# Kernel optimization log

Measured on AMD Instinct MI355X. Metric: run time of the kernel, lower is better.

Reference implementation:

```python
import jax, jax.numpy as jnp
import numpy as np

SEQ = 4096
EMBED = 1280
HEADS = 16
HEAD_DIM = EMBED // HEADS  # 80


def rotate_half(x):
    # interleaved rotate: out[..., 2i] = -x[..., 2i+1]; out[..., 2i+1] = x[..., 2i]
    x_even = x[..., ::2]
    x_odd = x[..., 1::2]
    return jnp.stack((-x_odd, x_even), axis=-1).reshape(x.shape)


def setup_inputs() -> dict:
    key = jax.random.key(0)
    ks = jax.random.split(key, 7)
    return {
        "hidden_states": jax.random.normal(ks[0], (SEQ, EMBED), dtype=jnp.float32),
        "cos": jax.random.uniform(ks[1], (SEQ, HEAD_DIM), dtype=jnp.float32),
        "sin": jax.random.uniform(ks[2], (SEQ, HEAD_DIM), dtype=jnp.float32),
        "w_qkv": jax.random.normal(ks[3], (EMBED, 3 * EMBED), dtype=jnp.float32) * 0.02,
        "b_qkv": jax.random.normal(ks[4], (3 * EMBED,), dtype=jnp.float32) * 0.02,
        "w_proj": jax.random.normal(ks[5], (EMBED, EMBED), dtype=jnp.float32) * 0.02,
        "b_proj": jax.random.normal(ks[6], (EMBED,), dtype=jnp.float32) * 0.02,
    }


def reference(hidden_states, cos, sin, w_qkv, b_qkv, w_proj, b_proj):
    S = hidden_states.shape[0]
    # QKV projection: (S, 3E) -> (S, 3, H, D)
    qkv = (hidden_states @ w_qkv + b_qkv).reshape(S, 3, HEADS, HEAD_DIM)
    q, k, v = qkv[:, 0], qkv[:, 1], qkv[:, 2]  # each (S, H, D)

    # RoPE in float32, cos/sin broadcast over heads: (S, 1, D)
    dt = q.dtype
    qf, kf = q.astype(jnp.float32), k.astype(jnp.float32)
    c = cos[:, None, :].astype(jnp.float32)
    s = sin[:, None, :].astype(jnp.float32)
    q = (qf * c + rotate_half(qf) * s).astype(dt)
    k = (kf * c + rotate_half(kf) * s).astype(dt)

    scaling = HEAD_DIM ** -0.5
    # attention scores per head: (H, S, S)
    scores = jnp.einsum("shd,thd->hst", q, k) * scaling
    attn = jax.nn.softmax(scores.astype(jnp.float32), axis=-1).astype(dt)
    # weighted values: (S, H, D)
    out = jnp.einsum("hst,thd->shd", attn, v).reshape(S, EMBED)
    return out @ w_proj + b_proj
```

## Files before the change

### kernel.cpp

```cpp
#include <hip/hip_runtime.h>
#include <hip/hip_bf16.h>

#define SEQ   4096
#define EMBED 1280
#define NH    16
#define HD    80
#define K1    EMBED
#define N1    (3*EMBED)

typedef short bfrag_t __attribute__((ext_vector_type(8)));
typedef float f32x4   __attribute__((ext_vector_type(4)));
typedef float f32x16  __attribute__((ext_vector_type(16)));

static __device__ __forceinline__ unsigned short f2bf(float x){
    __hip_bfloat16 h = __float2bfloat16(x);
    return __builtin_bit_cast(unsigned short, h);
}
static __device__ __forceinline__ float bf2f(unsigned short u){
    unsigned int v = ((unsigned int)u) << 16;
    return __builtin_bit_cast(float, v);
}

static __device__ __forceinline__ unsigned int pack2bf(float a, float b){
    unsigned int ua = __builtin_bit_cast(unsigned int, a) + 0x8000u;
    unsigned int ub = __builtin_bit_cast(unsigned int, b) + 0x8000u;
#if __has_builtin(__builtin_amdgcn_perm)
    return __builtin_amdgcn_perm(ub, ua, 0x07060302u);
#else
    return (ua >> 16) | (ub & 0xFFFF0000u);
#endif
}

static __device__ __forceinline__ float fast_exp2(float x){
#if __has_builtin(__builtin_amdgcn_exp2f)
    return __builtin_amdgcn_exp2f(x);
#else
    return __expf(x * 0.69314718056f);
#endif
}

static __device__ __forceinline__ void gload_lds16(const void* g, void* l){
#if __has_builtin(__builtin_amdgcn_global_load_lds)
    __builtin_amdgcn_global_load_lds(
        (const __attribute__((address_space(1))) unsigned int*)g,
        (__attribute__((address_space(3))) unsigned int*)l, 16, 0, 0);
#else
    *(uint4*)l = *(const uint4*)g;
#endif
}

static __device__ __forceinline__ bfrag_t ld_frag8(const unsigned short* p){
    uint2 lo = *(const uint2*)p;
    uint2 hi = *(const uint2*)(p + 4);
    uint4 u; u.x = lo.x; u.y = lo.y; u.z = hi.x; u.w = hi.y;
    return __builtin_bit_cast(bfrag_t, u);
}

#define CONV_BLOCKS (SEQ*EMBED/4/256)
#define TQ_BX (N1/32)
#define TQ_BLOCKS (TQ_BX*(K1/32))
#define TP_BX (EMBED/32)
#define TP_BLOCKS (TP_BX*(EMBED/32))

__global__ __launch_bounds__(256)
void prep_all(const float* __restrict__ hs, unsigned short* __restrict__ hb,
              const float* __restrict__ wqkv, unsigned short* __restrict__ wqT,
              const float* __restrict__ wproj, unsigned short* __restrict__ wpT)
{
    __shared__ float t[32][33];
    int b = blockIdx.x;
    if (b < CONV_BLOCKS){
        int i = b * 256 + threadIdx.x;
        float4 v = ((const float4*)hs)[i];
        ushort4 r;
        r.x = f2bf(v.x); r.y = f2bf(v.y); r.z = f2bf(v.z); r.w = f2bf(v.w);
        ((ushort4*)hb)[i] = r;
        return;
    }
    const float* in; unsigned short* outp; int R, C, bc, br;
    if (b < CONV_BLOCKS + TQ_BLOCKS){
        b -= CONV_BLOCKS;
        in = wqkv; outp = wqT; R = K1; C = N1;
        bc = (b % TQ_BX) * 32; br = (b / TQ_BX) * 32;
    } else {
        b -= CONV_BLOCKS + TQ_BLOCKS;
        in = wproj; outp = wpT; R = EMBED; C = EMBED;
        bc = (b % TP_BX) * 32; br = (b / TP_BX) * 32;
    }
    int tx = threadIdx.x & 31, ty = threadIdx.x >> 5;
    for (int i = ty; i < 32; i += 8) t[i][tx] = in[(size_t)(br + i) * C + bc + tx];
    __syncthreads();
    for (int i = ty; i < 32; i += 8) outp[(size_t)(bc + i) * R + br + tx] = f2bf(t[tx][i]);
}


__global__ __launch_bounds__(256, 4)
void gemm_qkv(const unsigned short* __restrict__ A,
              const unsigned short* __restrict__ BT,
              const float* __restrict__ bias,
              const float* __restrict__ cosp, const float* __restrict__ sinp,
              unsigned short* __restrict__ qout, unsigned short* __restrict__ kout,
              unsigned short* __restrict__ vout,
              int M, int N, int K)
{
    __shared__ union {
        struct { unsigned short A[128*32]; unsigned short B[128*32]; } ab;
        unsigned short tr[4][64][72];
    } lds;

    int tid  = threadIdx.x;
    int lane = tid & 63, wave = tid >> 6;
    int wm = wave >> 1, wn = wave & 1;
    int quad = lane >> 4, l16 = lane & 15;
    int m0 = blockIdx.y * 128, n0 = blockIdx.x * 128;

    f32x4 acc[4][4] = {};
    const unsigned short* ga = A  + (size_t)(m0 + (tid>>2)) * K + (tid&3)*8;
    const unsigned short* gb = BT + (size_t)(n0 + (tid>>2)) * K + (tid&3)*8;

    for (int k0 = 0; k0 < K; k0 += 32){
        __syncthreads();
        gload_lds16(ga,                &lds.ab.A[tid*8]);
        gload_lds16(ga + (size_t)64*K, &lds.ab.A[2048 + tid*8]);
        gload_lds16(gb,                &lds.ab.B[tid*8]);
        gload_lds16(gb + (size_t)64*K, &lds.ab.B[2048 + tid*8]);
        ga += 32; gb += 32;
        __syncthreads();
        bfrag_t af[4], bf[4];
        #pragma unroll
        for (int i = 0; i < 4; i++)
            af[i] = *(const bfrag_t*)&lds.ab.A[(wm*64 + i*16 + l16)*32 + quad*8];
        #pragma unroll
        for (int j = 0; j < 4; j++)
            bf[j] = *(const bfrag_t*)&lds.ab.B[(wn*64 + j*16 + l16)*32 + quad*8];
        #pragma unroll
        for (int i = 0; i < 4; i++)
            #pragma unroll
            for (int j = 0; j < 4; j++)
                acc[i][j] = __builtin_amdgcn_mfma_f32_16x16x32_bf16(af[i], bf[j], acc[i][j], 0, 0, 0);
    }

    const float scaling = 0.11180339887498949f;

    if (n0 >= 2*EMBED){
        __syncthreads();
        #pragma unroll
        for (int j = 0; j < 4; j++){
            int colw = j*16 + l16;
            float b = bias[n0 + wn*64 + colw];
            #pragma unroll
            for (int i = 0; i < 4; i++){
                ushort4 u;
                u.x = f2bf(acc[i][j][0] + b);
                u.y = f2bf(acc[i][j][1] + b);
                u.z = f2bf(acc[i][j][2] + b);
                u.w = f2bf(acc[i][j][3] + b);
                *(ushort4*)&lds.tr[wave][colw][i*16 + quad*4] = u;
            }
        }
        int c8 = lane >> 3, rc = lane & 7;
        #pragma unroll
        for (int cg = 0; cg < 8; cg++){
            int colw = cg*8 + c8;
            size_t colg = (size_t)(n0 - 2*EMBED) + wn*64 + colw;
            int rowg = m0 + wm*64 + rc*8;
            *(uint4*)&vout[colg*SEQ + rowg] = *(const uint4*)&lds.tr[wave][colw][rc*8];
        }
        return;
    }

    #pragma unroll
    for (int i = 0; i < 4; i++)
    #pragma unroll
    for (int j = 0; j < 4; j++){
        int colj  = n0 + wn*64 + j*16;
        int which = colj / EMBED;
        int rem   = colj - which*EMBED;
        int hh    = rem / HD;
        int dd    = rem - hh*HD;
        float b = bias[colj + l16];
        unsigned short* dst = (which == 0) ? qout : kout;
        float mult = (which == 0) ? scaling : 1.f;
        #pragma unroll
        for (int r = 0; r < 4; r++){
            int row = m0 + wm*64 + i*16 + quad*4 + r;
            float v = acc[i][j][r] + b;
            float vo = __shfl_xor(v, 1, 64);
            float c = cosp[(size_t)row*HD + dd + l16];
            float s = sinp[(size_t)row*HD + dd + l16];
            float o = (l16 & 1) ? (v*c + vo*s) : (v*c - vo*s);
            dst[((size_t)hh*SEQ + row)*HD + dd + l16] = f2bf(o * mult);
        }
    }
}


__global__ __launch_bounds__(256, 4)
void gemm_proj(const unsigned short* __restrict__ A,
               const unsigned short* __restrict__ BT,
               const float* __restrict__ bias,
               float* __restrict__ out,
               int M, int N, int K)
{
    __shared__ unsigned short As[64*32];
    __shared__ unsigned short Bs[128*32];
    int tid  = threadIdx.x;
    int lane = tid & 63, wave = tid >> 6;
    int wm = wave & 1, wn = wave >> 1;
    int quad = lane >> 4, l16 = lane & 15;
    int m0 = blockIdx.y * 64, n0 = blockIdx.x * 128;

    f32x4 acc[2][4] = {};
    const unsigned short* ga = A  + (size_t)(m0 + (tid>>2)) * K + (tid&3)*8;
    const unsigned short* gb = BT + (size_t)(n0 + (tid>>2)) * K + (tid&3)*8;

    for (int k0 = 0; k0 < K; k0 += 32){
        __syncthreads();
        gload_lds16(ga,                &As[tid*8]);
        gload_lds16(gb,                &Bs[tid*8]);
        gload_lds16(gb + (size_t)64*K, &Bs[2048 + tid*8]);
        ga += 32; gb += 32;
        __syncthreads();
        bfrag_t af[2], bf[4];
        #pragma unroll
        for (int i = 0; i < 2; i++)
            af[i] = *(const bfrag_t*)&As[(wm*32 + i*16 + l16)*32 + quad*8];
        #pragma unroll
        for (int j = 0; j < 4; j++)
            bf[j] = *(const bfrag_t*)&Bs[(wn*64 + j*16 + l16)*32 + quad*8];
        #pragma unroll
        for (int i = 0; i < 2; i++)
            #pragma unroll
            for (int j = 0; j < 4; j++)
                acc[i][j] = __builtin_amdgcn_mfma_f32_16x16x32_bf16(af[i], bf[j], acc[i][j], 0, 0, 0);
    }

    #pragma unroll
    for (int i = 0; i < 2; i++)
    #pragma unroll
    for (int j = 0; j < 4; j++){
        int col = n0 + wn*64 + j*16 + l16;
        float b = bias[col];
        #pragma unroll
        for (int r = 0; r < 4; r++){
            int row = m0 + wm*32 + i*16 + quad*4 + r;
            out[(size_t)row * N + col] = acc[i][j][r] + b;
        }
    }
}


__global__ __launch_bounds__(256, 4)
void attn_mfma(const unsigned short* __restrict__ q,
               const unsigned short* __restrict__ k,
               const unsigned short* __restrict__ vt,
               unsigned short* __restrict__ out,
               unsigned short* __restrict__ opart,
               float* __restrict__ lpart,
               int iters)
{
    __shared__ unsigned short Vt[2][80*64];
    __shared__ unsigned short Ps[128][68];

    int tid  = threadIdx.x;
    int lane = tid & 63, wave = tid >> 6;
    int quad = lane >> 4, l16 = lane & 15;
    int l32  = lane & 31, h2 = lane >> 5;
    int h = blockIdx.y, q0 = blockIdx.x * 128;
    int split = blockIdx.z;
    int kb0 = split * iters * 64;
    int qrow = wave*32 + l32;

    const unsigned short* qh = q  + ((size_t)h*SEQ + q0)*HD;
    const unsigned short* kh = k  + (size_t)h*SEQ*HD;
    const unsigned short* vh = vt + (size_t)h*HD*SEQ;

    bfrag_t qf[5];
    #pragma unroll
    for (int kk = 0; kk < 5; kk++)
        qf[kk] = *(const bfrag_t*)&qh[(size_t)qrow*HD + (kk*2 + h2)*8];

    auto stage = [&](int buf, int kb){
        unsigned short* dst = &Vt[buf][0];
        #pragma unroll
        for (int rnd = 0; rnd < 3; rnd++){
            int idx = rnd*256 + tid;
            if (rnd < 2 || tid < 128){
                int row = idx >> 3, c = idx & 7;
                gload_lds16(&vh[(size_t)row*SEQ + kb + ((c ^ (row & 7)) << 3)], &dst[idx*8]);
            }
        }
    };

    stage(0, kb0);

    float la = 0.f, lb = 0.f;
    f32x4 o_[2][5] = {};

    const unsigned short* kp = kh + (size_t)(kb0 + l32)*HD + h2*8;
    const float LOG2E = 1.44269504f;
    const float BIAS2 = -17.3123405f;

    for (int kt = 0; kt < iters; kt++){
        f32x16 S0 = {}, S1 = {};
        #pragma unroll
        for (int kk = 0; kk < 5; kk++){
            bfrag_t kf0 = *(const bfrag_t*)(kp + kk*16);
            bfrag_t kf1 = *(const bfrag_t*)(kp + (size_t)32*HD + kk*16);
            S0 = __builtin_amdgcn_mfma_f32_32x32x16_bf16(kf0, qf[kk], S0, 0,0,0);
            S1 = __builtin_amdgcn_mfma_f32_32x32x16_bf16(kf1, qf[kk], S1, 0,0,0);
        }
        kp += (size_t)64*HD;

        #pragma unroll
        for (int r = 0; r < 16; r++){
            float p0 = fast_exp2(fmaf(S0[r], LOG2E, BIAS2));
            float p1 = fast_exp2(fmaf(S1[r], LOG2E, BIAS2));
            S0[r] = p0; S1[r] = p1;
            la += p0; lb += p1;
        }

        #pragma unroll
        for (int g = 0; g < 4; g++){
            uint2 w0, w1;
            w0.x = pack2bf(S0[g*4+0], S0[g*4+1]);
            w0.y = pack2bf(S0[g*4+2], S0[g*4+3]);
            w1.x = pack2bf(S1[g*4+0], S1[g*4+1]);
            w1.y = pack2bf(S1[g*4+2], S1[g*4+3]);
            *(uint2*)&Ps[qrow][g*8 + h2*4]      = w0;
            *(uint2*)&Ps[qrow][32 + g*8 + h2*4] = w1;
        }

        __syncthreads();
        if (kt + 1 < iters) stage((kt+1)&1, kb0 + (kt+1)*64);

        int buf = kt & 1;
        #pragma unroll
        for (int kk = 0; kk < 2; kk++){
            bfrag_t pf0 = ld_frag8(&Ps[wave*32      + l16][kk*32 + quad*8]);
            bfrag_t pf1 = ld_frag8(&Ps[wave*32 + 16 + l16][kk*32 + quad*8]);
            #pragma unroll
            for (int dt = 0; dt < 5; dt++){
                int row = dt*16 + l16;
                bfrag_t vf = *(const bfrag_t*)&Vt[buf][row*64 + (((kk*4+quad) ^ (l16 & 7)) << 3)];
                o_[0][dt] = __builtin_amdgcn_mfma_f32_16x16x32_bf16(vf, pf0, o_[0][dt], 0,0,0);
                o_[1][dt] = __builtin_amdgcn_mfma_f32_16x16x32_bf16(vf, pf1, o_[1][dt], 0,0,0);
            }
        }
    }

    float l_ = la + lb;
    l_ += __shfl_xor(l_, 32, 64);

    if (gridDim.z == 1){
        #pragma unroll
        for (int i = 0; i < 2; i++){
            float linv = 1.f / __shfl(l_, i*16 + l16, 64);
            int qg = q0 + wave*32 + i*16 + l16;
            #pragma unroll
            for (int dt = 0; dt < 5; dt++){
                int d = dt*16 + quad*4;
                ushort4 u;
                u.x = f2bf(o_[i][dt][0]*linv);
                u.y = f2bf(o_[i][dt][1]*linv);
                u.z = f2bf(o_[i][dt][2]*linv);
                u.w = f2bf(o_[i][dt][3]*linv);
                *(ushort4*)&out[(size_t)qg*EMBED + h*HD + d] = u;
            }
        }
    } else {
        if (h2 == 0)
            lpart[((size_t)(split*NH + h))*SEQ + q0 + qrow] = l_;
        #pragma unroll
        for (int i = 0; i < 2; i++){
            int qg = q0 + wave*32 + i*16 + l16;
            size_t base = (((size_t)(split*NH + h))*SEQ + qg)*HD;
            #pragma unroll
            for (int dt = 0; dt < 5; dt++){
                int d = dt*16 + quad*4;
                ushort4 u;
                u.x = f2bf(o_[i][dt][0]);
                u.y = f2bf(o_[i][dt][1]);
                u.z = f2bf(o_[i][dt][2]);
                u.w = f2bf(o_[i][dt][3]);
                *(ushort4*)&opart[base + d] = u;
            }
        }
    }
}

__global__ __launch_bounds__(256)
void attn_combine(const unsigned short* __restrict__ op,
                  const float* __restrict__ lp,
                  unsigned short* __restrict__ out,
                  int ns)
{
    int t = blockIdx.x*256 + threadIdx.x;
    int d8 = t % 10;
    int qh = t / 10;
    int q  = qh & (SEQ-1);
    int h  = qh >> 12;
    float lsum = 0.f;
    for (int s = 0; s < ns; s++) lsum += lp[((size_t)(s*NH + h))*SEQ + q];
    float inv = 1.f / lsum;
    float acc[8] = {};
    for (int s = 0; s < ns; s++){
        uint4 A = *(const uint4*)&op[(((size_t)(s*NH + h))*SEQ + q)*HD + d8*8];
        unsigned int* a = (unsigned int*)&A;
        #pragma unroll
        for (int e = 0; e < 4; e++){
            acc[2*e]   += bf2f((unsigned short)(a[e] & 0xffff));
            acc[2*e+1] += bf2f((unsigned short)(a[e] >> 16));
        }
    }
    uint4 R;
    unsigned int* r = (unsigned int*)&R;
    #pragma unroll
    for (int e = 0; e < 4; e++)
        r[e] = pack2bf(acc[2*e]*inv, acc[2*e+1]*inv);
    *(uint4*)&out[(size_t)q*EMBED + h*HD + d8*8] = R;
}


extern "C" void kernel_launch(void* const* d_in, const int* in_sizes, int n_in,
                              void* d_out, int out_size, void* d_ws, size_t ws_size,
                              hipStream_t stream)
{
    const float* hs    = (const float*)d_in[0];
    const float* cosp  = (const float*)d_in[1];
    const float* sinp  = (const float*)d_in[2];
    const float* wqkv  = (const float*)d_in[3];
    const float* bqkv  = (const float*)d_in[4];
    const float* wproj = (const float*)d_in[5];
    const float* bproj = (const float*)d_in[6];
    float* out = (float*)d_out;

    char* ws = (char*)d_ws;
    size_t off = 0;
    auto alloc = [&](size_t bytes){ void* p = ws + off; off += bytes; return p; };
    unsigned short* hb    = (unsigned short*)alloc((size_t)SEQ*EMBED*2);
    unsigned short* wqT   = (unsigned short*)alloc((size_t)N1*K1*2);
    unsigned short* wpT   = (unsigned short*)alloc((size_t)EMBED*EMBED*2);
    unsigned short* q_ws  = (unsigned short*)alloc((size_t)SEQ*EMBED*2);
    unsigned short* k_ws  = (unsigned short*)alloc((size_t)SEQ*EMBED*2);
    unsigned short* v_ws  = (unsigned short*)alloc((size_t)SEQ*EMBED*2);
    unsigned short* a_ws  = (unsigned short*)alloc((size_t)SEQ*EMBED*2);
    size_t base = off;
    size_t per_split = (size_t)NH*SEQ*HD*2 + (size_t)NH*SEQ*4;
    int nsplit = 1;
    if (ws_size >= base + 4*per_split)      nsplit = 4;
    else if (ws_size >= base + 2*per_split) nsplit = 2;
    unsigned short* opart = (unsigned short*)alloc((size_t)nsplit*NH*SEQ*HD*2);
    float*          lpart = (float*)alloc((size_t)nsplit*NH*SEQ*4);

    prep_all<<<CONV_BLOCKS + TQ_BLOCKS + TP_BLOCKS, 256, 0, stream>>>(
        hs, hb, wqkv, wqT, wproj, wpT);

    gemm_qkv<<<dim3(N1/128, SEQ/128), 256, 0, stream>>>(
        hb, wqT, bqkv, cosp, sinp, q_ws, k_ws, v_ws, SEQ, N1, K1);

    attn_mfma<<<dim3(SEQ/128, NH, nsplit), 256, 0, stream>>>(
        q_ws, k_ws, v_ws, a_ws, opart, lpart, (SEQ/64)/nsplit);
    if (nsplit > 1)
        attn_combine<<<NH*SEQ*10/256, 256, 0, stream>>>(opart, lpart, a_ws, nsplit);

    gemm_proj<<<dim3(EMBED/128, SEQ/64), 256, 0, stream>>>(
        a_ws, wpT, bproj, out, SEQ, EMBED, EMBED);
}
```

Baseline: 322.6 us.

## Widen QKV GEMM K-tile to 64 with XOR-swizzled LDS, cap attention split at 2

The QKV GEMM now stages a 64-wide K slice per iteration instead of 32. This halves the number of barrier pairs, and an XOR swizzle on the LDS column index avoids bank conflicts on fragment reads. Separately, pack2bf uses the hardware packed bf16 conversion when available, and the attention split-K factor is capped at 2 instead of 4. Together these aim to cut GEMM synchronisation overhead and combine-kernel work. The trade-offs are doubled LDS use for the GEMM tiles, which may lower occupancy, and less parallelism in attention.

```diff
diff --git a/kernel.cpp b/kernel.cpp
--- a/kernel.cpp
+++ b/kernel.cpp
@@ -22,12 +22,17 @@
 }
 
 static __device__ __forceinline__ unsigned int pack2bf(float a, float b){
+#if __has_builtin(__builtin_amdgcn_cvt_pk_bf16_f32)
+    short2 p = __builtin_amdgcn_cvt_pk_bf16_f32(a, b);
+    return __builtin_bit_cast(unsigned int, p);
+#else
     unsigned int ua = __builtin_bit_cast(unsigned int, a) + 0x8000u;
     unsigned int ub = __builtin_bit_cast(unsigned int, b) + 0x8000u;
 #if __has_builtin(__builtin_amdgcn_perm)
     return __builtin_amdgcn_perm(ub, ua, 0x07060302u);
 #else
     return (ua >> 16) | (ub & 0xFFFF0000u);
+#endif
 #endif
 }
 
@@ -104,7 +109,7 @@
               int M, int N, int K)
 {
     __shared__ union {
-        struct { unsigned short A[128*32]; unsigned short B[128*32]; } ab;
+        struct { unsigned short A[128*64]; unsigned short B[128*64]; } ab;
         unsigned short tr[4][64][72];
     } lds;
 
@@ -114,30 +119,49 @@
     int quad = lane >> 4, l16 = lane & 15;
     int m0 = blockIdx.y * 128, n0 = blockIdx.x * 128;
 
+    const unsigned short* pa[4];
+    const unsigned short* pb[4];
+    int dsto[4];
+    #pragma unroll
+    for (int rnd = 0; rnd < 4; rnd++){
+        int idx = rnd*256 + tid;
+        int row = idx >> 3, c = idx & 7;
+        int cc = (c ^ (row & 7)) * 8;
+        pa[rnd] = A  + (size_t)(m0 + row) * K + cc;
+        pb[rnd] = BT + (size_t)(n0 + row) * K + cc;
+        dsto[rnd] = idx * 8;
+    }
+
     f32x4 acc[4][4] = {};
-    const unsigned short* ga = A  + (size_t)(m0 + (tid>>2)) * K + (tid&3)*8;
-    const unsigned short* gb = BT + (size_t)(n0 + (tid>>2)) * K + (tid&3)*8;
-
-    for (int k0 = 0; k0 < K; k0 += 32){
-        __syncthreads();
-        gload_lds16(ga,                &lds.ab.A[tid*8]);
-        gload_lds16(ga + (size_t)64*K, &lds.ab.A[2048 + tid*8]);
-        gload_lds16(gb,                &lds.ab.B[tid*8]);
-        gload_lds16(gb + (size_t)64*K, &lds.ab.B[2048 + tid*8]);
-        ga += 32; gb += 32;
-        __syncthreads();
-        bfrag_t af[4], bf[4];
-        #pragma unroll
-        for (int i = 0; i < 4; i++)
-            af[i] = *(const bfrag_t*)&lds.ab.A[(wm*64 + i*16 + l16)*32 + quad*8];
-        #pragma unroll
-        for (int j = 0; j < 4; j++)
-            bf[j] = *(const bfrag_t*)&lds.ab.B[(wn*64 + j*16 + l16)*32 + quad*8];
-        #pragma unroll
-        for (int i = 0; i < 4; i++)
-            #pragma unroll
-            for (int j = 0; j < 4; j++)
-                acc[i][j] = __builtin_amdgcn_mfma_f32_16x16x32_bf16(af[i], bf[j], acc[i][j], 0, 0, 0);
+
+    for (int k0 = 0; k0 < K; k0 += 64){
+        __syncthreads();
+        #pragma unroll
+        for (int rnd = 0; rnd < 4; rnd++){
+            gload_lds16(pa[rnd], &lds.ab.A[dsto[rnd]]);
+            gload_lds16(pb[rnd], &lds.ab.B[dsto[rnd]]);
+            pa[rnd] += 64; pb[rnd] += 64;
+        }
+        __syncthreads();
+        #pragma unroll
+        for (int kk = 0; kk < 2; kk++){
+            bfrag_t af[4], bf[4];
+            #pragma unroll
+            for (int i = 0; i < 4; i++){
+                int row = wm*64 + i*16 + l16;
+                af[i] = *(const bfrag_t*)&lds.ab.A[row*64 + (((kk*4+quad) ^ (l16 & 7)) << 3)];
+            }
+            #pragma unroll
+            for (int j = 0; j < 4; j++){
+                int row = wn*64 + j*16 + l16;
+                bf[j] = *(const bfrag_t*)&lds.ab.B[row*64 + (((kk*4+quad) ^ (l16 & 7)) << 3)];
+            }
+            #pragma unroll
+            for (int i = 0; i < 4; i++)
+                #pragma unroll
+                for (int j = 0; j < 4; j++)
+                    acc[i][j] = __builtin_amdgcn_mfma_f32_16x16x32_bf16(af[i], bf[j], acc[i][j], 0, 0, 0);
+        }
     }
 
     const float scaling = 0.11180339887498949f;
@@ -447,9 +471,7 @@
     unsigned short* a_ws  = (unsigned short*)alloc((size_t)SEQ*EMBED*2);
     size_t base = off;
     size_t per_split = (size_t)NH*SEQ*HD*2 + (size_t)NH*SEQ*4;
-    int nsplit = 1;
-    if (ws_size >= base + 4*per_split)      nsplit = 4;
-    else if (ws_size >= base + 2*per_split) nsplit = 2;
+    int nsplit = (ws_size >= base + 2*per_split) ? 2 : 1;
     unsigned short* opart = (unsigned short*)alloc((size_t)nsplit*NH*SEQ*HD*2);
     float*          lpart = (float*)alloc((size_t)nsplit*NH*SEQ*4);
 
```

Result: faster. 303.0 us (-6.1%).
